# Optimization experiments

Measured on AMD Instinct MI355X. Metric: run time of the kernel, lower is better.

The kernel has to match this reference:

```python
import jax, jax.numpy as jnp
import numpy as np

B, T, E = 4, 2048, 1024
H, D = 16, 64

def setup_inputs() -> dict:
    key = jax.random.key(0)
    k0, k1, k2, k3 = jax.random.split(key, 4)
    x = jax.random.normal(k0, (B, T, E), dtype=jnp.float32)
    Wq = jax.random.normal(k1, (H, E, D), dtype=jnp.float32) * (E ** -0.5)
    Wk = jax.random.normal(k2, (H, E, D), dtype=jnp.float32) * (E ** -0.5)
    Wv = jax.random.normal(k3, (H, E, D), dtype=jnp.float32) * (E ** -0.5)
    return {"x": x, "Wq": Wq, "Wk": Wk, "Wv": Wv}

def reference(x, Wq, Wk, Wv):
    # per-head projections: [B,T,E] x [H,E,D] -> [B,H,T,D]
    q = jnp.einsum('bte,hed->bhtd', x, Wq)
    k = jnp.einsum('bte,hed->bhtd', x, Wk)
    v = jnp.einsum('bte,hed->bhtd', x, Wv)
    d = q.shape[-1]
    scores = jnp.einsum('bhtd,bhsd->bhts', q, k) / jnp.sqrt(jnp.asarray(d, q.dtype))
    Tlen = x.shape[1]
    causal = jnp.tril(jnp.ones((Tlen, Tlen), dtype=bool))
    scores = jnp.where(causal, scores, -jnp.inf)
    weights = jax.nn.softmax(scores, axis=-1)
    out = jnp.einsum('bhts,bhsd->bhtd', weights, v)  # [B,H,T,D]
    # concat heads along last dim (head order preserved like torch.cat)
    Bb, Hh, Tt, Dd = out.shape
    return out.transpose(0, 2, 1, 3).reshape(Bb, Tt, Hh * Dd)
```

## Files before the change

kernel.cpp:

```cpp
#include <hip/hip_runtime.h>
#include <hip/hip_bf16.h>

#define BATCH 4
#define SEQ   2048
#define EMB   1024
#define NH    16
#define HD    64

#define Q_OFF  ((size_t)0)
#define K_OFF  ((size_t)8388608)
#define V_OFF  ((size_t)16777216)
#define WT_OFF ((size_t)25165824)

typedef __attribute__((ext_vector_type(8))) short short8;
typedef __attribute__((ext_vector_type(4))) short short4v;
typedef __attribute__((ext_vector_type(4))) float f32x4;

__device__ __forceinline__ short8 pack8s(float4 a, float4 b, float s) {
    alignas(16) __hip_bfloat16 t[8] = {
        __float2bfloat16(a.x * s), __float2bfloat16(a.y * s),
        __float2bfloat16(a.z * s), __float2bfloat16(a.w * s),
        __float2bfloat16(b.x * s), __float2bfloat16(b.y * s),
        __float2bfloat16(b.z * s), __float2bfloat16(b.w * s)};
    return *reinterpret_cast<const short8*>(t);
}

__device__ __forceinline__ void async16(void* lds, const void* g) {
    __builtin_amdgcn_global_load_lds(
        (const __attribute__((address_space(1))) unsigned int*)g,
        (__attribute__((address_space(3))) unsigned int*)lds, 16, 0, 0);
}

__global__ __launch_bounds__(256)
void xcast_kernel(const float* __restrict__ x, __hip_bfloat16* __restrict__ xb)
{
    const size_t i = ((size_t)blockIdx.x * 256 + threadIdx.x) * 8;
    float4 f0 = ((const float4*)(x + i))[0];
    float4 f1 = ((const float4*)(x + i))[1];
    *(short8*)(xb + i) = pack8s(f0, f1, 1.0f);
}

__global__ __launch_bounds__(256)
void wt_kernel(const float* __restrict__ Wq, const float* __restrict__ Wk,
               const float* __restrict__ Wv, __hip_bfloat16* __restrict__ Wt)
{
    const int et = blockIdx.x;
    const int mh = blockIdx.y;
    const int m = mh >> 4, h = mh & 15;
    const float* W = ((m == 0) ? Wq : (m == 1) ? Wk : Wv) + (size_t)h * (EMB * HD);
    const float scale = (m == 0) ? 0.18033688011112042f : 1.0f;

    __shared__ __hip_bfloat16 T[64][72];
    const int tid = threadIdx.x;
    const int r   = tid >> 2;
    const int seg = (tid & 3) * 16;

    {
        const float* src = W + (size_t)(et * 64 + r) * HD + seg;
        float4 f0 = ((const float4*)src)[0];
        float4 f1 = ((const float4*)src)[1];
        float4 f2 = ((const float4*)src)[2];
        float4 f3 = ((const float4*)src)[3];
        const float v[16] = {f0.x,f0.y,f0.z,f0.w, f1.x,f1.y,f1.z,f1.w,
                             f2.x,f2.y,f2.z,f2.w, f3.x,f3.y,f3.z,f3.w};
        #pragma unroll
        for (int j = 0; j < 16; ++j) T[seg + j][r] = __float2bfloat16(v[j] * scale);
    }
    __syncthreads();
    __hip_bfloat16* dst = Wt + ((size_t)mh * HD + r) * EMB + et * 64 + seg;
    *(short8*)dst       = *(const short8*)&T[r][seg];
    *(short8*)(dst + 8) = *(const short8*)&T[r][seg + 8];
}

__global__ __launch_bounds__(256)
void qkv_proj_kernel(const __hip_bfloat16* __restrict__ xb,
                     const __hip_bfloat16* __restrict__ Wt,
                     __hip_bfloat16* __restrict__ qkv)
{
    const int nt = blockIdx.x;
    const int rt = blockIdx.y;
    const int row0 = rt * 128;
    const int n0   = nt * 128;

    __shared__ __hip_bfloat16 lds[17408];
    __hip_bfloat16* As = lds;
    __hip_bfloat16* Bs = lds + 8192;

    const int tid  = threadIdx.x;
    const int wave = tid >> 6;
    const int lane = tid & 63;
    const int lr   = lane & 15;
    const int lg   = lane >> 4;

    const int srow  = lane >> 3;
    const int sslot = (lane & 7) ^ srow;
    const char* aSrc = (const char*)xb + (size_t)(row0 + wave * 32 + srow) * 2048 + sslot * 16;
    const char* bSrc = (const char*)Wt + (size_t)(n0   + wave * 32 + srow) * 2048 + sslot * 16;
    char* aDst = (char*)As + (size_t)(wave * 32) * 128;
    char* bDst = (char*)Bs + (size_t)(wave * 32) * 128;

    f32x4 acc[2][8] = {};

    for (int k0 = 0; k0 < EMB; k0 += 64) {
        __syncthreads();
        #pragma unroll
        for (int i = 0; i < 4; ++i) {
            async16(aDst + i * 1024, aSrc + (size_t)i * 16384 + k0 * 2);
            async16(bDst + i * 1024, bSrc + (size_t)i * 16384 + k0 * 2);
        }
        __syncthreads();

        #pragma unroll
        for (int half = 0; half < 2; ++half) {
            const int cg = half * 4 + lg;
            const int r0a = wave * 32 + lr;
            const int r1a = wave * 32 + 16 + lr;
            short8 a0 = *(const short8*)((char*)As + r0a * 128 + ((cg ^ (r0a & 7)) * 16));
            short8 a1 = *(const short8*)((char*)As + r1a * 128 + ((cg ^ (r1a & 7)) * 16));
            #pragma unroll
            for (int ct = 0; ct < 8; ++ct) {
                const int rb = ct * 16 + lr;
                short8 bf = *(const short8*)((char*)Bs + rb * 128 + ((cg ^ (rb & 7)) * 16));
                acc[0][ct] = __builtin_amdgcn_mfma_f32_16x16x32_bf16(a0, bf, acc[0][ct], 0, 0, 0);
                acc[1][ct] = __builtin_amdgcn_mfma_f32_16x16x32_bf16(a1, bf, acc[1][ct], 0, 0, 0);
            }
        }
    }

    const int m   = n0 >> 10;
    const int b   = row0 >> 11;
    const int tl0 = (row0 & (SEQ - 1)) + wave * 32;
    if (m < 2) {
        __hip_bfloat16* outp = qkv + ((m == 0) ? Q_OFF : K_OFF)
                             + (size_t)b * NH * SEQ * HD;
        #pragma unroll
        for (int rsub = 0; rsub < 2; ++rsub)
            #pragma unroll
            for (int ct = 0; ct < 8; ++ct) {
                const int h = (2 * nt + (ct >> 2)) & 15;
                const int d = (ct & 3) * 16 + lr;
                #pragma unroll
                for (int i = 0; i < 4; ++i) {
                    const int trow = tl0 + rsub * 16 + lg * 4 + i;
                    outp[((size_t)h * SEQ + trow) * HD + d] = __float2bfloat16(acc[rsub][ct][i]);
                }
            }
    } else {
        __hip_bfloat16 (*Ts)[136] = (__hip_bfloat16(*)[136])lds;
        __syncthreads();
        #pragma unroll
        for (int rsub = 0; rsub < 2; ++rsub)
            #pragma unroll
            for (int ct = 0; ct < 8; ++ct)
                #pragma unroll
                for (int i = 0; i < 4; ++i)
                    Ts[ct * 16 + lr][wave * 32 + rsub * 16 + lg * 4 + i] =
                        __float2bfloat16(acc[rsub][ct][i]);
        __syncthreads();
        const int c    = tid >> 1;
        const int tseg = (tid & 1) * 64;
        const int hv   = (2 * nt + (c >> 6)) & 15;
        const int dv   = c & 63;
        __hip_bfloat16* dst = qkv + V_OFF + ((size_t)b * NH + hv) * (HD * SEQ)
                            + (size_t)dv * SEQ + (row0 & (SEQ - 1)) + tseg;
        #pragma unroll
        for (int q = 0; q < 8; ++q)
            *(short8*)(dst + q * 8) = *(const short8*)&Ts[c][tseg + q * 8];
    }
}

__global__ __launch_bounds__(256)
void attn_kernel(const __hip_bfloat16* __restrict__ ws, float* __restrict__ out)
{
    const int bid = blockIdx.x;
    const int qt  = 15 - (bid >> 6);
    const int bh  = bid & 63;
    const int h   = bh & 15;
    const int b   = bh >> 4;
    const int qbase = qt * 128;
    const int ktmax = 2 * qt + 1;

    const __hip_bfloat16* qp = ws + Q_OFF + (size_t)bh * (SEQ * HD);
    const __hip_bfloat16* kp = ws + K_OFF + (size_t)bh * (SEQ * HD);
    const __hip_bfloat16* vt = ws + V_OFF + (size_t)bh * (HD * SEQ);

    __shared__ __align__(16) __hip_bfloat16 Ksb[2][4096];
    __shared__ __align__(16) __hip_bfloat16 Vsb[2][4096];
    __shared__ __align__(16) __hip_bfloat16 Psb[4][1024];

    const int tid  = threadIdx.x;
    const int wave = tid >> 6;
    const int lane = tid & 63;
    const int lr   = lane & 15;
    const int lg   = lane >> 4;
    const int l7   = lr & 7;

    const int srow8 = lane >> 3;
    const int sslot = (lane & 7) ^ srow8;

    short8 qf[2][2];
    #pragma unroll
    for (int rsub = 0; rsub < 2; ++rsub) {
        const __hip_bfloat16* src =
            qp + (size_t)(qbase + wave * 32 + rsub * 16 + lr) * HD + lg * 8;
        qf[rsub][0] = *(const short8*)src;
        qf[rsub][1] = *(const short8*)(src + 32);
    }

    float m_run[2] = {-1e30f, -1e30f};
    float l_run[2] = {0.f, 0.f};
    f32x4 o_acc[2][4] = {};

    auto stage = [&](int buf, int kbase) {
        #pragma unroll
        for (int j = 0; j < 2; ++j) {
            const int r0 = wave * 16 + j * 8;
            async16((char*)Ksb[buf] + r0 * 128,
                    (const char*)(kp + (size_t)(kbase + r0 + srow8) * HD) + sslot * 16);
            async16((char*)Vsb[buf] + r0 * 128,
                    (const char*)(vt + (size_t)(r0 + srow8) * SEQ + kbase) + sslot * 16);
        }
    };

    stage(0, 0);
    __syncthreads();

    for (int kt = 0; kt <= ktmax; ++kt) {
        const int cur = kt & 1;
        if (kt < ktmax) stage(cur ^ 1, (kt + 1) * 64);

        f32x4 s[2][4];
        __builtin_amdgcn_s_setprio(1);
        #pragma unroll
        for (int ct = 0; ct < 4; ++ct) {
            const char* kb = (const char*)Ksb[cur] + (ct * 16 + lr) * 128;
            short8 kf0 = *(const short8*)(kb + ((lg      ^ l7) << 4));
            short8 kf1 = *(const short8*)(kb + (((lg + 4) ^ l7) << 4));
            #pragma unroll
            for (int rsub = 0; rsub < 2; ++rsub) {
                f32x4 z = {};
                z           = __builtin_amdgcn_mfma_f32_16x16x32_bf16(kf0, qf[rsub][0], z, 0, 0, 0);
                s[rsub][ct] = __builtin_amdgcn_mfma_f32_16x16x32_bf16(kf1, qf[rsub][1], z, 0, 0, 0);
            }
        }
        __builtin_amdgcn_s_setprio(0);

        const int kbase = kt * 64;
        if (kt >= 2 * qt) {
            #pragma unroll
            for (int rsub = 0; rsub < 2; ++rsub) {
                const int qrow = qbase + wave * 32 + rsub * 16 + lr;
                #pragma unroll
                for (int ct = 0; ct < 4; ++ct)
                    #pragma unroll
                    for (int i = 0; i < 4; ++i) {
                        const int key = kbase + ct * 16 + lg * 4 + i;
                        s[rsub][ct][i] = (key > qrow) ? -1e30f : s[rsub][ct][i];
                    }
            }
        }

        short8 pf[2][2];
        #pragma unroll
        for (int rsub = 0; rsub < 2; ++rsub) {
            float pmax = fmaxf(
                fmaxf(fmaxf(fmaxf(s[rsub][0][0], s[rsub][0][1]), fmaxf(s[rsub][0][2], s[rsub][0][3])),
                      fmaxf(fmaxf(s[rsub][1][0], s[rsub][1][1]), fmaxf(s[rsub][1][2], s[rsub][1][3]))),
                fmaxf(fmaxf(fmaxf(s[rsub][2][0], s[rsub][2][1]), fmaxf(s[rsub][2][2], s[rsub][2][3])),
                      fmaxf(fmaxf(s[rsub][3][0], s[rsub][3][1]), fmaxf(s[rsub][3][2], s[rsub][3][3]))));
            pmax = fmaxf(pmax, __shfl_xor(pmax, 16, 64));
            pmax = fmaxf(pmax, __shfl_xor(pmax, 32, 64));

            if (__any(pmax > m_run[rsub] + 8.0f)) {
                const float mnew = fmaxf(m_run[rsub], pmax);
                const float corr = __builtin_amdgcn_exp2f(m_run[rsub] - mnew);
                l_run[rsub] *= corr;
                #pragma unroll
                for (int ct = 0; ct < 4; ++ct)
                    #pragma unroll
                    for (int i = 0; i < 4; ++i)
                        o_acc[rsub][ct][i] *= corr;
                m_run[rsub] = mnew;
            }

            const float mcur = m_run[rsub];
            float rs0 = 0.f, rs1 = 0.f;
            #pragma unroll
            for (int ct = 0; ct < 4; ++ct) {
                const float p0 = __builtin_amdgcn_exp2f(s[rsub][ct][0] - mcur);
                const float p1 = __builtin_amdgcn_exp2f(s[rsub][ct][1] - mcur);
                const float p2 = __builtin_amdgcn_exp2f(s[rsub][ct][2] - mcur);
                const float p3 = __builtin_amdgcn_exp2f(s[rsub][ct][3] - mcur);
                rs0 += p0 + p1;
                rs1 += p2 + p3;
                alignas(8) __hip_bfloat16 t[4] = {
                    __float2bfloat16(p0), __float2bfloat16(p1),
                    __float2bfloat16(p2), __float2bfloat16(p3)};
                *(short4v*)((char*)Psb[wave] + lr * 128
                    + (((2 * ct + (lg >> 1)) ^ l7) << 4) + 8 * (lg & 1)) = *(const short4v*)t;
            }
            float rs = rs0 + rs1;
            rs += __shfl_xor(rs, 16, 64);
            rs += __shfl_xor(rs, 32, 64);
            l_run[rsub] += rs;

            const char* pb = (const char*)Psb[wave] + lr * 128;
            pf[rsub][0] = *(const short8*)(pb + ((lg      ^ l7) << 4));
            pf[rsub][1] = *(const short8*)(pb + (((lg + 4) ^ l7) << 4));
        }

        __builtin_amdgcn_s_setprio(1);
        #pragma unroll
        for (int ct = 0; ct < 4; ++ct) {
            const char* vb = (const char*)Vsb[cur] + (ct * 16 + lr) * 128;
            short8 vf0 = *(const short8*)(vb + ((lg      ^ l7) << 4));
            short8 vf1 = *(const short8*)(vb + (((lg + 4) ^ l7) << 4));
            #pragma unroll
            for (int rsub = 0; rsub < 2; ++rsub) {
                o_acc[rsub][ct] = __builtin_amdgcn_mfma_f32_16x16x32_bf16(vf0, pf[rsub][0], o_acc[rsub][ct], 0, 0, 0);
                o_acc[rsub][ct] = __builtin_amdgcn_mfma_f32_16x16x32_bf16(vf1, pf[rsub][1], o_acc[rsub][ct], 0, 0, 0);
            }
        }
        __builtin_amdgcn_s_setprio(0);

        __syncthreads();
    }

    float* op = out + (size_t)b * SEQ * (NH * HD) + (size_t)h * HD;
    #pragma unroll
    for (int rsub = 0; rsub < 2; ++rsub) {
        const float inv  = 1.0f / l_run[rsub];
        const int   trow = qbase + wave * 32 + rsub * 16 + lr;
        #pragma unroll
        for (int ct = 0; ct < 4; ++ct) {
            float4 o;
            o.x = o_acc[rsub][ct][0] * inv;
            o.y = o_acc[rsub][ct][1] * inv;
            o.z = o_acc[rsub][ct][2] * inv;
            o.w = o_acc[rsub][ct][3] * inv;
            *(float4*)&op[(size_t)trow * (NH * HD) + ct * 16 + lg * 4] = o;
        }
    }
}

extern "C" void kernel_launch(void* const* d_in, const int* in_sizes, int n_in,
                              void* d_out, int out_size, void* d_ws, size_t ws_size,
                              hipStream_t stream) {
    const float* x  = (const float*)d_in[0];
    const float* Wq = (const float*)d_in[1];
    const float* Wk = (const float*)d_in[2];
    const float* Wv = (const float*)d_in[3];
    float* out = (float*)d_out;
    __hip_bfloat16* ws = (__hip_bfloat16*)d_ws;

    __hip_bfloat16* xb = (__hip_bfloat16*)d_out;

    hipLaunchKernelGGL(xcast_kernel, dim3((BATCH * SEQ * EMB) / (256 * 8)), dim3(256),
                       0, stream, x, xb);
    hipLaunchKernelGGL(wt_kernel, dim3(16, 48), dim3(256), 0, stream,
                       Wq, Wk, Wv, ws + WT_OFF);
    hipLaunchKernelGGL(qkv_proj_kernel, dim3(24, 64), dim3(256), 0, stream,
                       xb, ws + WT_OFF, ws);
    hipLaunchKernelGGL(attn_kernel, dim3(1024), dim3(256), 0, stream, ws, out);
}
```

Measured before the change: 155.6 us.

## Split causal attention along keys with paired query tiles and a combine pass

Replaces the single attention kernel with a split-K variant. Each block pairs query tile qt with tile 15-qt and handles half of each tile's key range, so every block does the same amount of work. Partial bf16 outputs plus their running max and sum go to workspace, and a separate combine kernel rescales and merges the two halves into the fp32 output. This adds a kernel launch, extra global traffic for the partials and a bf16 rounding of the unnormalized partial outputs. It falls back to the old kernel when the workspace is too small.

```diff
diff --git a/kernel.cpp b/kernel.cpp
--- a/kernel.cpp
+++ b/kernel.cpp
@@ -11,6 +11,11 @@
 #define K_OFF  ((size_t)8388608)
 #define V_OFF  ((size_t)16777216)
 #define WT_OFF ((size_t)25165824)
+
+#define PO_BYTE ((size_t)50331648)
+#define PM_BYTE (PO_BYTE + (size_t)33554432)
+#define PL_BYTE (PM_BYTE + (size_t)1048576)
+#define WS_NEED (PL_BYTE + (size_t)1048576)
 
 typedef __attribute__((ext_vector_type(8))) short short8;
 typedef __attribute__((ext_vector_type(4))) short short4v;
@@ -170,6 +175,244 @@
 }
 
 __global__ __launch_bounds__(256)
+void attn_splitk_kernel(const __hip_bfloat16* __restrict__ ws, char* __restrict__ part)
+{
+    const int bid = blockIdx.x;
+    const int bh  = bid & 63;
+    const int j   = bid >> 6;
+    const int jq  = j & 7;
+    const int jh  = j >> 3;
+
+    const __hip_bfloat16* qp = ws + Q_OFF + (size_t)bh * (SEQ * HD);
+    const __hip_bfloat16* kp = ws + K_OFF + (size_t)bh * (SEQ * HD);
+    const __hip_bfloat16* vt = ws + V_OFF + (size_t)bh * (HD * SEQ);
+
+    __hip_bfloat16* Po = (__hip_bfloat16*)(part + PO_BYTE);
+    float*          Pm = (float*)(part + PM_BYTE);
+    float*          Pl = (float*)(part + PL_BYTE);
+
+    __shared__ __align__(16) __hip_bfloat16 Ksb[2][4096];
+    __shared__ __align__(16) __hip_bfloat16 Vsb[2][4096];
+    __shared__ __align__(16) __hip_bfloat16 Psb[4][1024];
+
+    const int tid  = threadIdx.x;
+    const int wave = tid >> 6;
+    const int lane = tid & 63;
+    const int lr   = lane & 15;
+    const int lg   = lane >> 4;
+    const int l7   = lr & 7;
+
+    const int srow8 = lane >> 3;
+    const int sslot = (lane & 7) ^ srow8;
+
+    auto stage = [&](int buf, int kbase) {
+        #pragma unroll
+        for (int jj = 0; jj < 2; ++jj) {
+            const int r0 = wave * 16 + jj * 8;
+            async16((char*)Ksb[buf] + r0 * 128,
+                    (const char*)(kp + (size_t)(kbase + r0 + srow8) * HD) + sslot * 16);
+            async16((char*)Vsb[buf] + r0 * 128,
+                    (const char*)(vt + (size_t)(r0 + srow8) * SEQ + kbase) + sslot * 16);
+        }
+    };
+
+    for (int sidx = 0; sidx < 2; ++sidx) {
+        const int qt    = sidx ? (7 - jq) : (8 + jq);
+        const int cnt   = qt + 1;
+        const int kt0   = jh * cnt;
+        const int qbase = qt * 128;
+
+        short8 qf[2][2];
+        #pragma unroll
+        for (int rsub = 0; rsub < 2; ++rsub) {
+            const __hip_bfloat16* src =
+                qp + (size_t)(qbase + wave * 32 + rsub * 16 + lr) * HD + lg * 8;
+            qf[rsub][0] = *(const short8*)src;
+            qf[rsub][1] = *(const short8*)(src + 32);
+        }
+
+        float m_run[2] = {-1e30f, -1e30f};
+        float l_run[2] = {0.f, 0.f};
+        f32x4 o_acc[2][4] = {};
+
+        stage(0, kt0 * 64);
+        __syncthreads();
+
+        for (int kk = 0; kk < cnt; ++kk) {
+            const int kt  = kt0 + kk;
+            const int cur = kk & 1;
+            if (kk + 1 < cnt) stage(cur ^ 1, (kt + 1) * 64);
+
+            f32x4 s[2][4];
+            __builtin_amdgcn_s_setprio(1);
+            #pragma unroll
+            for (int ct = 0; ct < 4; ++ct) {
+                const char* kb = (const char*)Ksb[cur] + (ct * 16 + lr) * 128;
+                short8 kf0 = *(const short8*)(kb + ((lg      ^ l7) << 4));
+                short8 kf1 = *(const short8*)(kb + (((lg + 4) ^ l7) << 4));
+                #pragma unroll
+                for (int rsub = 0; rsub < 2; ++rsub) {
+                    f32x4 z = {};
+                    z           = __builtin_amdgcn_mfma_f32_16x16x32_bf16(kf0, qf[rsub][0], z, 0, 0, 0);
+                    s[rsub][ct] = __builtin_amdgcn_mfma_f32_16x16x32_bf16(kf1, qf[rsub][1], z, 0, 0, 0);
+                }
+            }
+            __builtin_amdgcn_s_setprio(0);
+
+            const int kbase = kt * 64;
+            if (kt >= 2 * qt) {
+                #pragma unroll
+                for (int rsub = 0; rsub < 2; ++rsub) {
+                    const int qrow = qbase + wave * 32 + rsub * 16 + lr;
+                    #pragma unroll
+                    for (int ct = 0; ct < 4; ++ct)
+                        #pragma unroll
+                        for (int i = 0; i < 4; ++i) {
+                            const int key = kbase + ct * 16 + lg * 4 + i;
+                            s[rsub][ct][i] = (key > qrow) ? -3.0e38f : s[rsub][ct][i];
+                        }
+                }
+            }
+
+            short8 pf[2][2];
+            #pragma unroll
+            for (int rsub = 0; rsub < 2; ++rsub) {
+                float pmax = fmaxf(
+                    fmaxf(fmaxf(fmaxf(s[rsub][0][0], s[rsub][0][1]), fmaxf(s[rsub][0][2], s[rsub][0][3])),
+                          fmaxf(fmaxf(s[rsub][1][0], s[rsub][1][1]), fmaxf(s[rsub][1][2], s[rsub][1][3]))),
+                    fmaxf(fmaxf(fmaxf(s[rsub][2][0], s[rsub][2][1]), fmaxf(s[rsub][2][2], s[rsub][2][3])),
+                          fmaxf(fmaxf(s[rsub][3][0], s[rsub][3][1]), fmaxf(s[rsub][3][2], s[rsub][3][3]))));
+                pmax = fmaxf(pmax, __shfl_xor(pmax, 16, 64));
+                pmax = fmaxf(pmax, __shfl_xor(pmax, 32, 64));
+
+                if (__any(pmax > m_run[rsub] + 8.0f)) {
+                    const float mnew = fmaxf(m_run[rsub], pmax);
+                    const float corr = __builtin_amdgcn_exp2f(m_run[rsub] - mnew);
+                    l_run[rsub] *= corr;
+                    #pragma unroll
+                    for (int ct = 0; ct < 4; ++ct)
+                        #pragma unroll
+                        for (int i = 0; i < 4; ++i)
+                            o_acc[rsub][ct][i] *= corr;
+                    m_run[rsub] = mnew;
+                }
+
+                const float mcur = m_run[rsub];
+                float rs0 = 0.f, rs1 = 0.f;
+                #pragma unroll
+                for (int ct = 0; ct < 4; ++ct) {
+                    const float p0 = __builtin_amdgcn_exp2f(s[rsub][ct][0] - mcur);
+                    const float p1 = __builtin_amdgcn_exp2f(s[rsub][ct][1] - mcur);
+                    const float p2 = __builtin_amdgcn_exp2f(s[rsub][ct][2] - mcur);
+                    const float p3 = __builtin_amdgcn_exp2f(s[rsub][ct][3] - mcur);
+                    rs0 += p0 + p1;
+                    rs1 += p2 + p3;
+                    alignas(8) __hip_bfloat16 t[4] = {
+                        __float2bfloat16(p0), __float2bfloat16(p1),
+                        __float2bfloat16(p2), __float2bfloat16(p3)};
+                    *(short4v*)((char*)Psb[wave] + lr * 128
+                        + (((2 * ct + (lg >> 1)) ^ l7) << 4) + 8 * (lg & 1)) = *(const short4v*)t;
+                }
+                float rs = rs0 + rs1;
+                rs += __shfl_xor(rs, 16, 64);
+                rs += __shfl_xor(rs, 32, 64);
+                l_run[rsub] += rs;
+
+                const char* pb = (const char*)Psb[wave] + lr * 128;
+                pf[rsub][0] = *(const short8*)(pb + ((lg      ^ l7) << 4));
+                pf[rsub][1] = *(const short8*)(pb + (((lg + 4) ^ l7) << 4));
+            }
+
+            __builtin_amdgcn_s_setprio(1);
+            #pragma unroll
+            for (int ct = 0; ct < 4; ++ct) {
+                const char* vb = (const char*)Vsb[cur] + (ct * 16 + lr) * 128;
+                short8 vf0 = *(const short8*)(vb + ((lg      ^ l7) << 4));
+                short8 vf1 = *(const short8*)(vb + (((lg + 4) ^ l7) << 4));
+                #pragma unroll
+                for (int rsub = 0; rsub < 2; ++rsub) {
+                    o_acc[rsub][ct] = __builtin_amdgcn_mfma_f32_16x16x32_bf16(vf0, pf[rsub][0], o_acc[rsub][ct], 0, 0, 0);
+                    o_acc[rsub][ct] = __builtin_amdgcn_mfma_f32_16x16x32_bf16(vf1, pf[rsub][1], o_acc[rsub][ct], 0, 0, 0);
+                }
+            }
+            __builtin_amdgcn_s_setprio(0);
+
+            __syncthreads();
+        }
+
+        const int slot = (bh * 16 + qt) * 2 + jh;
+        __hip_bfloat16* po = Po + (size_t)slot * 8192;
+        #pragma unroll
+        for (int rsub = 0; rsub < 2; ++rsub) {
+            const int rloc = wave * 32 + rsub * 16 + lr;
+            #pragma unroll
+            for (int ct = 0; ct < 4; ++ct) {
+                alignas(8) __hip_bfloat16 t[4] = {
+                    __float2bfloat16(o_acc[rsub][ct][0]),
+                    __float2bfloat16(o_acc[rsub][ct][1]),
+                    __float2bfloat16(o_acc[rsub][ct][2]),
+                    __float2bfloat16(o_acc[rsub][ct][3])};
+                *(short4v*)(po + (size_t)rloc * 64 + ct * 16 + lg * 4) = *(const short4v*)t;
+            }
+            if (lg == 0) {
+                Pm[slot * 128 + rloc] = m_run[rsub];
+                Pl[slot * 128 + rloc] = l_run[rsub];
+            }
+        }
+    }
+}
+
+__global__ __launch_bounds__(256)
+void combine_kernel(const char* __restrict__ part, float* __restrict__ out)
+{
+    const int idx = blockIdx.x;
+    const int bh  = idx >> 4;
+    const int qt  = idx & 15;
+    const int h   = bh & 15;
+    const int b   = bh >> 4;
+
+    const __hip_bfloat16* Po = (const __hip_bfloat16*)(part + PO_BYTE);
+    const float*          Pm = (const float*)(part + PM_BYTE);
+    const float*          Pl = (const float*)(part + PL_BYTE);
+    const int s0 = idx * 2, s1 = idx * 2 + 1;
+
+    const int tid = threadIdx.x;
+    const int row = tid >> 1;
+    const int d0  = (tid & 1) * 32;
+
+    const float m0 = Pm[s0 * 128 + row], m1 = Pm[s1 * 128 + row];
+    const float l0 = Pl[s0 * 128 + row], l1 = Pl[s1 * 128 + row];
+    const float mm = fmaxf(m0, m1);
+    const float w0 = __builtin_amdgcn_exp2f(m0 - mm);
+    const float w1 = __builtin_amdgcn_exp2f(m1 - mm);
+    const float inv = 1.0f / (w0 * l0 + w1 * l1);
+    const float a0 = w0 * inv, a1 = w1 * inv;
+
+    const __hip_bfloat16* p0 = Po + ((size_t)s0 * 128 + row) * 64 + d0;
+    const __hip_bfloat16* p1 = Po + ((size_t)s1 * 128 + row) * 64 + d0;
+    float* op = out + ((size_t)b * SEQ + qt * 128 + row) * (NH * HD) + h * HD + d0;
+
+    #pragma unroll
+    for (int q = 0; q < 4; ++q) {
+        short8 av = ((const short8*)p0)[q];
+        short8 cv = ((const short8*)p1)[q];
+        const __hip_bfloat16* ab = (const __hip_bfloat16*)&av;
+        const __hip_bfloat16* cb = (const __hip_bfloat16*)&cv;
+        float4 r0, r1;
+        r0.x = a0 * __bfloat162float(ab[0]) + a1 * __bfloat162float(cb[0]);
+        r0.y = a0 * __bfloat162float(ab[1]) + a1 * __bfloat162float(cb[1]);
+        r0.z = a0 * __bfloat162float(ab[2]) + a1 * __bfloat162float(cb[2]);
+        r0.w = a0 * __bfloat162float(ab[3]) + a1 * __bfloat162float(cb[3]);
+        r1.x = a0 * __bfloat162float(ab[4]) + a1 * __bfloat162float(cb[4]);
+        r1.y = a0 * __bfloat162float(ab[5]) + a1 * __bfloat162float(cb[5]);
+        r1.z = a0 * __bfloat162float(ab[6]) + a1 * __bfloat162float(cb[6]);
+        r1.w = a0 * __bfloat162float(ab[7]) + a1 * __bfloat162float(cb[7]);
+        ((float4*)op)[q * 2]     = r0;
+        ((float4*)op)[q * 2 + 1] = r1;
+    }
+}
+
+__global__ __launch_bounds__(256)
 void attn_kernel(const __hip_bfloat16* __restrict__ ws, float* __restrict__ out)
 {
     const int bid = blockIdx.x;
@@ -213,8 +456,8 @@
 
     auto stage = [&](int buf, int kbase) {
         #pragma unroll
-        for (int j = 0; j < 2; ++j) {
-            const int r0 = wave * 16 + j * 8;
+        for (int jj = 0; jj < 2; ++jj) {
+            const int r0 = wave * 16 + jj * 8;
             async16((char*)Ksb[buf] + r0 * 128,
                     (const char*)(kp + (size_t)(kbase + r0 + srow8) * HD) + sslot * 16);
             async16((char*)Vsb[buf] + r0 * 128,
@@ -361,5 +604,13 @@
                        Wq, Wk, Wv, ws + WT_OFF);
     hipLaunchKernelGGL(qkv_proj_kernel, dim3(24, 64), dim3(256), 0, stream,
                        xb, ws + WT_OFF, ws);
-    hipLaunchKernelGGL(attn_kernel, dim3(1024), dim3(256), 0, stream, ws, out);
-}
+
+    if (ws_size >= WS_NEED) {
+        hipLaunchKernelGGL(attn_splitk_kernel, dim3(1024), dim3(256), 0, stream,
+                           ws, (char*)d_ws);
+        hipLaunchKernelGGL(combine_kernel, dim3(1024), dim3(256), 0, stream,
+                           (const char*)d_ws, out);
+    } else {
+        hipLaunchKernelGGL(attn_kernel, dim3(1024), dim3(256), 0, stream, ws, out);
+    }
+}
```

After: 175.9 us. +13.1%, slower.
